# Optimization experiments

Measured on AMD Instinct MI355X. Metric: run time of the kernel, lower is better.

Reference implementation:

```python
import jax, jax.numpy as jnp
import numpy as np

DIM = 256
FEATURE_SCALE = 4
NMS_THRESHOLD = 8.0
PRE_NMS_TOPK = 2048
MAX_OUTPUT = 256
MIN_SCORE = 0.2


def conv3d_same(x, w, b):
    # x: [D,H,W,Cin], w: [3,3,3,Cin,Cout] -> [D,H,W,Cout], SAME padding (flax default)
    y = jax.lax.conv_general_dilated(
        x[None], w, window_strides=(1, 1, 1), padding="SAME",
        dimension_numbers=("NDHWC", "DHWIO", "NDHWC"))
    return y[0] + b


def setup_inputs() -> dict:
    key = jax.random.key(0)
    ks = jax.random.split(key, 8)
    D, H, W, C = 16, 64, 64, 256
    feature = jax.random.normal(ks[0], (D, H, W, C), jnp.float32)
    mask = jax.random.bernoulli(ks[1], 0.8, (D * FEATURE_SCALE, H * FEATURE_SCALE, W * FEATURE_SCALE))
    s3a = 1.0 / np.sqrt(27 * C)
    s3b = 1.0 / np.sqrt(27 * DIM)
    s1 = 1.0 / np.sqrt(DIM)
    w0 = jax.random.normal(ks[2], (3, 3, 3, C, DIM), jnp.float32) * s3a
    b0 = jnp.zeros((DIM,), jnp.float32)
    w1 = jax.random.normal(ks[3], (3, 3, 3, DIM, DIM), jnp.float32) * s3b
    b1 = jnp.zeros((DIM,), jnp.float32)
    w_logit = jax.random.normal(ks[4], (DIM, 1), jnp.float32) * s1
    b_logit = jnp.zeros((1,), jnp.float32)
    w_reg = jax.random.normal(ks[5], (DIM, 3), jnp.float32) * s1
    b_reg = jnp.zeros((3,), jnp.float32)
    return dict(feature=feature, mask=mask, w0=w0, b0=b0, w1=w1, b1=b1,
                w_logit=w_logit, b_logit=b_logit, w_reg=w_reg, b_reg=b_reg)


def reference(feature, mask, w0, b0, w1, b1, w_logit, b_logit, w_reg, b_reg):
    # ---- feature mixing: n_layers=2 of conv3d + gelu (flax gelu is approximate/tanh) ----
    x = jax.nn.gelu(conv3d_same(feature, w0, b0))
    x = jax.nn.gelu(conv3d_same(x, w1, b1))
    D, H, W = x.shape[:3]

    # ---- detection block: 1x1 convs are pointwise dense layers ----
    logits = (x @ w_logit + b_logit)[..., 0].reshape(-1)          # [N]
    regressions = (x @ w_reg + b_reg)                              # [D,H,W,3]
    ref_locs = (jnp.moveaxis(jnp.mgrid[:D, :H, :W], 0, -1) + 0.5) * FEATURE_SCALE
    pred_locs = (ref_locs + regressions * FEATURE_SCALE).reshape(-1, 3)  # [N,3]

    # ---- generate_predictions: sigmoid scores, pre-NMS top-k, greedy distance NMS ----
    scores = jax.nn.sigmoid(logits)
    top_scores, idx = jax.lax.top_k(scores, PRE_NMS_TOPK)          # sorted desc
    top_locs = pred_locs[idx]                                      # [K,3]
    d2 = ((top_locs[:, None, :] - top_locs[None, :, :]) ** 2).sum(-1)  # [K,K]
    th2 = NMS_THRESHOLD * NMS_THRESHOLD

    def step(suppressed, i):
        keep_i = (~suppressed[i]) & (top_scores[i] >= MIN_SCORE)
        suppressed = suppressed | (keep_i & (d2[i] < th2))
        return suppressed, keep_i

    _, keep = jax.lax.scan(step, jnp.zeros((PRE_NMS_TOPK,), bool), jnp.arange(PRE_NMS_TOPK))
    sel_scores = jnp.where(keep, top_scores, 0.0)
    out_scores, oidx = jax.lax.top_k(sel_scores, MAX_OUTPUT)       # [M]
    out_locs = top_locs[oidx]                                      # [M,3]

    # ---- mask gather: floor/clip/index, zero out-of-mask scores ----
    pli = jnp.floor(out_locs).astype(jnp.int32)
    bound = jnp.array(mask.shape, jnp.int32) - 1
    plc = jnp.clip(pli, 0, bound)
    in_range = (pli == plc).all(axis=1)
    masked = jnp.where(in_range, mask[plc[:, 0], plc[:, 1], plc[:, 2]], False)
    out_scores = jnp.where(masked, out_scores, 0.0)

    return jnp.concatenate([out_locs, out_scores[:, None]], axis=-1)  # [M,4] = (z,y,x,score)
```

## Files before the change

kernel.cpp:

```cpp
#include <hip/hip_runtime.h>
#include <math.h>

#define Dz 16
#define Hy 64
#define Wx 64
#define CHN 256
#define NVOX (Dz*Hy*Wx)
#define TOPK 2048
#define MAXOUT 256
#define CAND_CAP 4096
#define NBCAP 16
#define NHIST 65536

typedef __attribute__((ext_vector_type(8))) _Float16 h8;
typedef __attribute__((ext_vector_type(8))) unsigned short u16x8;
typedef __attribute__((ext_vector_type(4))) float f32x4;

__device__ __forceinline__ float gelu_tanh(float x) {
    return 0.5f*x*(1.0f + tanhf(0.7978845608028654f*(x + 0.044715f*x*x*x)));
}
__device__ __forceinline__ unsigned f2sort(float f) {
    unsigned u = __float_as_uint(f);
    return (u & 0x80000000u) ? ~u : (u | 0x80000000u);
}
__device__ __forceinline__ float sort2f(unsigned s) {
    unsigned u = (s & 0x80000000u) ? (s & 0x7fffffffu) : ~s;
    return __uint_as_float(u);
}

#define MFMA(d, a, b) d = __builtin_amdgcn_mfma_f32_16x16x32_f16(a, b, d, 0, 0, 0)

__global__ __launch_bounds__(256) void prep_kernel(const float* __restrict__ w0,
        const float* __restrict__ w1, u16x8* __restrict__ wpk0,
        u16x8* __restrict__ wpk1, unsigned* __restrict__ hist,
        unsigned* __restrict__ counter) {
    int b = blockIdx.x, t = threadIdx.x;
    if (b < 1728) {
        int id = b*256 + t;
        int l = (id >= 221184) ? 1 : 0;
        int r = id - l*221184;
        int lane = r & 63, ng = (r >> 6) & 15, kbg = (r >> 10) & 7, tp = r >> 13;
        const float* w = l ? w1 : w0;
        u16x8* dst = l ? wpk1 : wpk0;
        h8 hv, lv;
        #pragma unroll
        for (int j = 0; j < 8; ++j) {
            int k = kbg*32 + (lane >> 4)*8 + j;
            int co = ng*16 + (lane & 15);
            float v = w[((size_t)tp*CHN + k)*CHN + co];
            _Float16 h = (_Float16)v;
            hv[j] = h;
            lv[j] = (_Float16)(v - (float)h);
        }
        size_t base = (((size_t)(tp*8 + kbg)*16 + ng)*2)*64 + lane;
        dst[base]      = __builtin_bit_cast(u16x8, hv);
        dst[base + 64] = __builtin_bit_cast(u16x8, lv);
    } else {
        int zb = b - 1728;
        int i = zb*256 + t;
        hist[i] = 0u; hist[i + 16384] = 0u; hist[i + 32768] = 0u; hist[i + 49152] = 0u;
        if (zb == 0 && t == 0) counter[0] = 0u;
    }
}

template<int LAYER>
__global__ __launch_bounds__(512, 4) void conv_kernel(
        const float* __restrict__ fsrc,
        const unsigned short* __restrict__ hhi, const unsigned short* __restrict__ hlo,
        const u16x8* __restrict__ wpk, const float* __restrict__ bias,
        unsigned short* __restrict__ ohi, unsigned short* __restrict__ olo,
        const float* __restrict__ wlog, const float* __restrict__ blog,
        const float* __restrict__ wreg, const float* __restrict__ breg,
        float* __restrict__ locs, unsigned long long* __restrict__ keys,
        unsigned* __restrict__ hist) {
    __shared__ h8 sm[4224];
    const int tid = threadIdx.x;
    const int lane = tid & 63, w = tid >> 6;
    const int yo = w >> 2, wn = w & 3;
    const int lr = lane & 15, lg = lane >> 4;
    const int z = blockIdx.y, y0 = blockIdx.x*2;

    f32x4 acc[4][4];
    #pragma unroll
    for (int m = 0; m < 4; ++m)
        #pragma unroll
        for (int n = 0; n < 4; ++n) acc[m][n] = (f32x4){0.f,0.f,0.f,0.f};

    for (int dz = 0; dz < 3; ++dz) {
        const int zz = z + dz - 1;
        for (int kc = 0; kc < 4; ++kc) {
            __syncthreads();
            if (LAYER == 0) {
                for (int cidx = tid; cidx < 2112; cidx += 512) {
                    int cd = cidx & 7;
                    int rr = cidx >> 3;
                    int r = rr % 66, iy = rr / 66;
                    int ygl = y0 - 1 + iy, xin = r - 1;
                    h8 hv = {0,0,0,0,0,0,0,0}, lv = {0,0,0,0,0,0,0,0};
                    if (((unsigned)zz < (unsigned)Dz) & ((unsigned)ygl < (unsigned)Hy)
                        & ((unsigned)xin < (unsigned)Wx)) {
                        const float* s = fsrc + ((size_t)((zz*Hy + ygl)*Wx + xin))*CHN
                                              + kc*64 + cd*8;
                        float4 t0 = *(const float4*)s;
                        float4 t1 = *(const float4*)(s + 4);
                        float vv[8] = {t0.x,t0.y,t0.z,t0.w,t1.x,t1.y,t1.z,t1.w};
                        #pragma unroll
                        for (int j = 0; j < 8; ++j) {
                            _Float16 h = (_Float16)vv[j];
                            hv[j] = h;
                            lv[j] = (_Float16)(vv[j] - (float)h);
                        }
                    }
                    int sl = cd ^ (r & 7);
                    sm[(iy*66 + r)*8 + sl] = hv;
                    sm[2112 + (iy*66 + r)*8 + sl] = lv;
                }
            } else {
                for (int cidx = tid; cidx < 4224; cidx += 512) {
                    int c = cidx & 7;
                    int rr = cidx >> 3;
                    int r = rr % 66, tt = rr / 66;
                    int p = tt >> 2, iy = tt & 3;
                    int ygl = y0 - 1 + iy, xin = r - 1;
                    u16x8 v = {0,0,0,0,0,0,0,0};
                    if (((unsigned)zz < (unsigned)Dz) & ((unsigned)ygl < (unsigned)Hy)
                        & ((unsigned)xin < (unsigned)Wx)) {
                        const unsigned short* bp = p ? hlo : hhi;
                        v = *(const u16x8*)(bp + ((size_t)((zz*Hy + ygl)*Wx + xin))*CHN
                                               + kc*64 + (size_t)((c ^ (r & 7)))*8);
                    }
                    sm[cidx] = __builtin_bit_cast(h8, v);
                }
            }
            __syncthreads();
            for (int dy = 0; dy < 3; ++dy) {
                const int iyA = yo + dy;
                const h8* As = sm + iyA*528;
                #pragma unroll
                for (int dx = 0; dx < 3; ++dx) {
                    const int tap = (dz*3 + dy)*3 + dx;
                    #pragma unroll
                    for (int kb = 0; kb < 2; ++kb) {
                        const int kbg = kc*2 + kb;
                        const u16x8* wb = wpk + ((size_t)(tap*8 + kbg)*32 + wn*8)*64 + lane;
                        h8 bh[4];
                        #pragma unroll
                        for (int n = 0; n < 4; ++n)
                            bh[n] = __builtin_bit_cast(h8, wb[(size_t)n*128]);
                        #pragma unroll
                        for (int m = 0; m < 4; ++m) {
                            const int r = m*16 + lr + dx;
                            const int sl = (kb*4 + lg) ^ (r & 7);
                            h8 ah = As[r*8 + sl];
                            h8 al = As[2112 + r*8 + sl];
                            #pragma unroll
                            for (int n = 0; n < 4; ++n) {
                                MFMA(acc[m][n], ah, bh[n]);
                                MFMA(acc[m][n], al, bh[n]);
                            }
                        }
                        h8 bl[4];
                        #pragma unroll
                        for (int n = 0; n < 4; ++n)
                            bl[n] = __builtin_bit_cast(h8, wb[(size_t)n*128 + 64]);
                        #pragma unroll
                        for (int m = 0; m < 4; ++m) {
                            const int r = m*16 + lr + dx;
                            const int sl = (kb*4 + lg) ^ (r & 7);
                            h8 ah = As[r*8 + sl];
                            #pragma unroll
                            for (int n = 0; n < 4; ++n) MFMA(acc[m][n], ah, bl[n]);
                        }
                    }
                }
            }
        }
    }

    float bn[4];
    #pragma unroll
    for (int n = 0; n < 4; ++n) bn[n] = bias[wn*64 + n*16 + lr];

    if (LAYER == 0) {
        const int ygl = y0 + yo;
        #pragma unroll
        for (int m = 0; m < 4; ++m) {
            #pragma unroll
            for (int rg = 0; rg < 4; ++rg) {
                const int x = m*16 + lg*4 + rg;
                const size_t vbase = ((size_t)((z*Hy + ygl)*Wx + x))*CHN;
                #pragma unroll
                for (int n = 0; n < 4; ++n) {
                    const int co = wn*64 + n*16 + lr;
                    float g = gelu_tanh(acc[m][n][rg] + bn[n]);
                    _Float16 h = (_Float16)g;
                    _Float16 l = (_Float16)(g - (float)h);
                    ohi[vbase + co] = __builtin_bit_cast(unsigned short, h);
                    olo[vbase + co] = __builtin_bit_cast(unsigned short, l);
                }
            }
        }
    } else {
        float wl[4], wr0[4], wr1[4], wr2[4];
        #pragma unroll
        for (int n = 0; n < 4; ++n) {
            const int co = wn*64 + n*16 + lr;
            wl[n] = wlog[co];
            wr0[n] = wreg[co*3 + 0]; wr1[n] = wreg[co*3 + 1]; wr2[n] = wreg[co*3 + 2];
        }
        float p[4][16];
        #pragma unroll
        for (int c = 0; c < 4; ++c)
            #pragma unroll
            for (int xi = 0; xi < 16; ++xi) p[c][xi] = 0.f;
        #pragma unroll
        for (int m = 0; m < 4; ++m)
            #pragma unroll
            for (int rg = 0; rg < 4; ++rg) {
                const int xi = m*4 + rg;
                #pragma unroll
                for (int n = 0; n < 4; ++n) {
                    float g = gelu_tanh(acc[m][n][rg] + bn[n]);
                    p[0][xi] += g*wl[n];
                    p[1][xi] += g*wr0[n];
                    p[2][xi] += g*wr1[n];
                    p[3][xi] += g*wr2[n];
                }
            }
        #pragma unroll
        for (int st = 0; st < 4; ++st) {
            const int s = 1 << st;
            #pragma unroll
            for (int c = 0; c < 4; ++c)
                #pragma unroll
                for (int xi = 0; xi < 16; ++xi)
                    p[c][xi] += __shfl_xor(p[c][xi], s, 64);
        }
        __syncthreads();
        float* det = (float*)sm;
        if (lr == 0) {
            #pragma unroll
            for (int m = 0; m < 4; ++m)
                #pragma unroll
                for (int rg = 0; rg < 4; ++rg) {
                    const int x = m*16 + lg*4 + rg;
                    #pragma unroll
                    for (int c = 0; c < 4; ++c)
                        det[((yo*64 + x)*4 + c)*4 + wn] = p[c][m*4 + rg];
                }
        }
        __syncthreads();
        {
            const int yo2 = tid >> 8, x = (tid >> 2) & 63, chn = tid & 3;
            const float* dp = det + ((yo2*64 + x)*4 + chn)*4;
            float s = dp[0] + dp[1] + dp[2] + dp[3];
            const int ygl = y0 + yo2;
            const int vg = (z*Hy + ygl)*Wx + x;
            if (chn == 0) {
                float logit = s + blog[0];
                float score = 1.f/(1.f + expf(-logit));
                unsigned sb = f2sort(score);
                keys[vg] = ((unsigned long long)sb << 32)
                         | (unsigned long long)(0xFFFFFFFFu - (unsigned)vg);
                atomicAdd(&hist[sb >> 16], 1u);
            } else {
                float coord = (chn == 1) ? (float)z : (chn == 2) ? (float)ygl : (float)x;
                float loc = (coord + 0.5f)*4.0f + (s + breg[chn-1])*4.0f;
                locs[(size_t)vg*3 + (chn-1)] = loc;
            }
        }
    }
}

__global__ __launch_bounds__(1024) void find_cut_kernel(const unsigned* __restrict__ hist,
                                                        unsigned* __restrict__ cutp) {
    __shared__ unsigned ps[1024];
    __shared__ unsigned fs[64];
    __shared__ int sh_cb;
    __shared__ unsigned sh_acc;
    int t = threadIdx.x;
    unsigned s = 0;
    const unsigned* hp = hist + (size_t)t*64;
    for (int j = 0; j < 64; ++j) s += hp[j];
    ps[t] = s;
    __syncthreads();
    for (int off = 1; off < 1024; off <<= 1) {
        unsigned v = ps[t] + ((t + off < 1024) ? ps[t + off] : 0u);
        __syncthreads();
        ps[t] = v;
        __syncthreads();
    }
    if (ps[t] >= TOPK && (t == 1023 || ps[t+1] < TOPK)) {
        sh_cb = t; sh_acc = (t == 1023) ? 0u : ps[t+1];
    }
    __syncthreads();
    int cb = sh_cb; unsigned acc = sh_acc;
    if (t < 64) {
        unsigned f = acc;
        for (int u = t; u < 64; ++u) f += hist[(size_t)cb*64 + u];
        fs[t] = f;
    }
    __syncthreads();
    if (t < 64) {
        if (fs[t] >= TOPK && (t == 63 || fs[t+1] < TOPK))
            cutp[0] = ((unsigned)(cb*64 + t)) << 16;
    }
}

__global__ void compact_kernel(const unsigned long long* __restrict__ keys,
                               const unsigned* __restrict__ cutp,
                               unsigned* __restrict__ counter,
                               unsigned long long* __restrict__ cand) {
    int i = blockIdx.x*blockDim.x + threadIdx.x;
    unsigned thr = cutp[0];
    unsigned long long k = keys[i];
    if ((unsigned)(k >> 32) >= thr) {
        unsigned p = atomicAdd(counter, 1u);
        if (p < CAND_CAP) cand[p] = k;
    }
}

__global__ __launch_bounds__(128) void rank_kernel(const unsigned* __restrict__ counter,
        const unsigned long long* __restrict__ cand, const float* __restrict__ locs,
        float4* __restrict__ loc4G) {
    __shared__ unsigned long long kbuf[CAND_CAP];
    int t = threadIdx.x;
    int g = blockIdx.x*128 + t;
    int M = (int)*counter; if (M > CAND_CAP) M = CAND_CAP;
    for (int i = t; i < CAND_CAP; i += 128) kbuf[i] = (i < M) ? cand[i] : 0ull;
    __syncthreads();
    if (g >= M) return;
    unsigned long long mykey = kbuf[g];
    int rank = 0;
    for (int j = 0; j < M; ++j) rank += (kbuf[j] > mykey) ? 1 : 0;
    if (rank < TOPK) {
        unsigned idx = 0xFFFFFFFFu - (unsigned)(mykey & 0xFFFFFFFFull);
        float4 v;
        v.x = locs[(size_t)idx*3 + 0];
        v.y = locs[(size_t)idx*3 + 1];
        v.z = locs[(size_t)idx*3 + 2];
        v.w = sort2f((unsigned)(mykey >> 32));
        loc4G[rank] = v;
    }
}

__global__ __launch_bounds__(64) void nbr_kernel(const float4* __restrict__ loc4G,
        unsigned short* __restrict__ nbidx, unsigned char* __restrict__ nbcnt) {
    __shared__ float4 b4[TOPK];
    int t = threadIdx.x;
    int g = blockIdx.x*64 + t;
    for (int i = t; i < TOPK; i += 64) b4[i] = loc4G[i];
    __syncthreads();
    float4 me = b4[g];
    int cnt = 0;
    for (int j = 0; j < TOPK; ++j) {
        float4 o = b4[j];
        float dz = o.x - me.x, dy = o.y - me.y, dx = o.z - me.z;
        float d2 = dz*dz + dy*dy + dx*dx;
        if (d2 < 64.0f && j != g) {
            if (cnt < NBCAP) nbidx[(size_t)g*NBCAP + cnt] = (unsigned short)j;
            cnt++;
        }
    }
    nbcnt[g] = (unsigned char)min(cnt, 255);
}

__global__ __launch_bounds__(512) void nms_kernel(const float4* __restrict__ loc4G,
        const unsigned short* __restrict__ nbidx, const unsigned char* __restrict__ nbcnt,
        const int* __restrict__ mask, float* __restrict__ out) {
    __shared__ float4 p4[TOPK];
    __shared__ unsigned short snb[TOPK*NBCAP];
    __shared__ unsigned char scnt[TOPK];
    __shared__ unsigned char supf[TOPK];
    __shared__ unsigned char keepB[TOPK];
    __shared__ unsigned keepw[64];
    __shared__ int wpre[64];
    __shared__ int sh_nk;
    int t = threadIdx.x;
    for (int i = t; i < TOPK; i += 512) {
        p4[i] = loc4G[i]; scnt[i] = nbcnt[i]; supf[i] = 0; keepB[i] = 0;
    }
    for (int i = t; i < TOPK*NBCAP/8; i += 512)
        ((uint4*)snb)[i] = ((const uint4*)nbidx)[i];
    __syncthreads();
    if (t < 64) {
        const int l = t;
        float cz[32], cy[32], cx[32];
        #pragma unroll
        for (int j = 0; j < 32; ++j) {
            float4 v = p4[l*32 + j];
            cz[j] = v.x; cy[j] = v.y; cx[j] = v.z;
        }
        int myok = 0;
        #pragma unroll
        for (int j = 0; j < 32; ++j) myok += (p4[l*32 + j].w >= 0.2f) ? 1 : 0;
        #pragma unroll
        for (int s = 1; s < 64; s <<= 1) myok += __shfl_xor(myok, s, 64);
        const int NS = myok;
        int keeps = 0;
        for (int i = 0; i < NS; ++i) {
            bool kept = (supf[i] == 0);
            if (kept) {
                if (l == 0) keepB[i] = 1;
                ++keeps;
                const int cnt = scnt[i];
                if (cnt <= NBCAP) {
                    if (l < cnt) supf[snb[i*NBCAP + l]] = 1;
                } else {
                    float4 pv = p4[i];
                    #pragma unroll
                    for (int j = 0; j < 32; ++j) {
                        float dz = cz[j]-pv.x, dy = cy[j]-pv.y, dx = cx[j]-pv.z;
                        if (dz*dz + dy*dy + dx*dx < 64.0f) supf[l*32 + j] = 1;
                    }
                }
                asm volatile("s_waitcnt lgkmcnt(0)" ::: "memory");
                if (keeps >= MAXOUT) break;
            }
        }
    }
    __syncthreads();
    if (t < 64) {
        unsigned wmask = 0u;
        for (int j = 0; j < 32; ++j) wmask |= (keepB[t*32 + j] ? 1u : 0u) << j;
        keepw[t] = wmask;
    }
    __syncthreads();
    if (t < 64) {
        int p = 0;
        for (int j = 0; j < t; ++j) p += __popc(keepw[j]);
        wpre[t] = p;
        if (t == 63) sh_nk = p + __popc(keepw[63]);
    }
    __syncthreads();
    const int nk = sh_nk;
    for (int i = t; i < TOPK; i += 512) {
        unsigned w = keepw[i >> 5];
        bool kp = (w >> (i & 31)) & 1u;
        int rk = wpre[i >> 5] + __popc(w & ((1u << (i & 31)) - 1u));
        int slot = kp ? rk : (nk + (i - rk));
        if (slot < MAXOUT) {
            float4 v = p4[i];
            float lz = v.x, ly = v.y, lx = v.z;
            float sc = kp ? v.w : 0.f;
            int iz = (int)floorf(lz), iy = (int)floorf(ly), ix = (int)floorf(lx);
            int cz2 = min(max(iz,0),Dz*4-1), cy2 = min(max(iy,0),Hy*4-1), cx2 = min(max(ix,0),Wx*4-1);
            bool inr = (iz==cz2) && (iy==cy2) && (ix==cx2);
            float osc = (inr && mask[((size_t)cz2*(Hy*4) + cy2)*(Wx*4) + cx2] != 0) ? sc : 0.f;
            out[slot*4+0] = lz; out[slot*4+1] = ly; out[slot*4+2] = lx; out[slot*4+3] = osc;
        }
    }
}

extern "C" void kernel_launch(void* const* d_in, const int* in_sizes, int n_in,
                              void* d_out, int out_size, void* d_ws, size_t ws_size,
                              hipStream_t stream) {
    const float* feature = (const float*)d_in[0];
    const int*   mask    = (const int*)d_in[1];
    const float* w0   = (const float*)d_in[2];
    const float* b0   = (const float*)d_in[3];
    const float* w1   = (const float*)d_in[4];
    const float* b1   = (const float*)d_in[5];
    const float* wlog = (const float*)d_in[6];
    const float* blog = (const float*)d_in[7];
    const float* wreg = (const float*)d_in[8];
    const float* breg = (const float*)d_in[9];

    char* ws = (char*)d_ws;
    size_t off = 0;
    unsigned short* h1hi = (unsigned short*)(ws + off); off += (size_t)NVOX*CHN*2;
    unsigned short* h1lo = (unsigned short*)(ws + off); off += (size_t)NVOX*CHN*2;
    u16x8* wpk0 = (u16x8*)(ws + off);               off += (size_t)442368*16;
    u16x8* wpk1 = (u16x8*)(ws + off);               off += (size_t)442368*16;
    unsigned long long* keys = (unsigned long long*)(ws + off); off += (size_t)NVOX*8;
    float* locs = (float*)(ws + off);               off += (size_t)NVOX*3*4;
    unsigned* hist = (unsigned*)(ws + off);         off += (size_t)NHIST*4;
    unsigned* counter = (unsigned*)(ws + off);      off += 256;
    unsigned* cutp = counter + 1;
    unsigned long long* cand = (unsigned long long*)(ws + off); off += (size_t)CAND_CAP*8;
    float4* loc4G = (float4*)(ws + off);            off += (size_t)TOPK*16;
    unsigned short* nbidx = (unsigned short*)(ws + off); off += (size_t)TOPK*NBCAP*2;
    unsigned char* nbcnt = (unsigned char*)(ws + off);   off += (size_t)TOPK;
    if (ws_size < off) return;

    prep_kernel<<<1792, 256, 0, stream>>>(w0, w1, wpk0, wpk1, hist, counter);
    dim3 cgrid(Hy/2, Dz);
    conv_kernel<0><<<cgrid, 512, 0, stream>>>(feature, nullptr, nullptr, wpk0, b0,
                                              h1hi, h1lo,
                                              nullptr, nullptr, nullptr, nullptr,
                                              nullptr, nullptr, nullptr);
    conv_kernel<1><<<cgrid, 512, 0, stream>>>(nullptr, h1hi, h1lo, wpk1, b1,
                                              nullptr, nullptr,
                                              wlog, blog, wreg, breg,
                                              locs, keys, hist);
    find_cut_kernel<<<1, 1024, 0, stream>>>(hist, cutp);
    compact_kernel<<<NVOX/256, 256, 0, stream>>>(keys, cutp, counter, cand);
    rank_kernel<<<CAND_CAP/128, 128, 0, stream>>>(counter, cand, locs, loc4G);
    nbr_kernel<<<TOPK/64, 64, 0, stream>>>(loc4G, nbidx, nbcnt);
    nms_kernel<<<1, 512, 0, stream>>>(loc4G, nbidx, nbcnt, mask, (float*)d_out);
}
```

Measured before the change: 1.382 ms.

## Double-buffer conv input tiles in LDS and widen blocks to 1024 threads

The conv kernels now use two LDS buffers. The next (dz, kc) input chunk is prefetched into registers while MFMAs run on the current buffer, then written to the other buffer, so only one barrier is needed per stage. Blocks grow to 1024 threads (16 waves), each wave covering 32 output channels instead of 64. This halves per-wave accumulators but doubles LDS use and doubles how often each A fragment is re-read across waves. The detection reduction is adjusted to sum over 8 channel groups.

After: 1.373 ms (median of 2 runs). Within noise of the previous version (-0.6%).

```diff
diff --git a/kernel.cpp b/kernel.cpp
--- a/kernel.cpp
+++ b/kernel.cpp
@@ -63,8 +63,51 @@
     }
 }
 
+__device__ __forceinline__ u16x8 ld1(int cidx, const unsigned short* __restrict__ hhi,
+        const unsigned short* __restrict__ hlo, int zz, bool zok, int y0, int kc) {
+    int c = cidx & 7, rr = cidx >> 3;
+    int r = rr % 66, tt = rr / 66;
+    int p = tt >> 2, iy = tt & 3;
+    int ygl = y0 - 1 + iy, xin = r - 1;
+    u16x8 v = {0,0,0,0,0,0,0,0};
+    if (zok & ((unsigned)ygl < (unsigned)Hy) & ((unsigned)xin < (unsigned)Wx)) {
+        const unsigned short* bp = p ? hlo : hhi;
+        v = *(const u16x8*)(bp + ((size_t)((zz*Hy + ygl)*Wx + xin))*CHN
+                            + kc*64 + (size_t)(c ^ (r & 7))*8);
+    }
+    return v;
+}
+__device__ __forceinline__ void ld0(int cidx, const float* __restrict__ fsrc,
+        int zz, bool zok, int y0, int kc, float4& va, float4& vb) {
+    int cd = cidx & 7, rr = cidx >> 3;
+    int r = rr % 66, iy = rr / 66;
+    int ygl = y0 - 1 + iy, xin = r - 1;
+    va = make_float4(0.f,0.f,0.f,0.f); vb = va;
+    if (zok & ((unsigned)ygl < (unsigned)Hy) & ((unsigned)xin < (unsigned)Wx)) {
+        const float* s = fsrc + ((size_t)((zz*Hy + ygl)*Wx + xin))*CHN + kc*64 + cd*8;
+        va = *(const float4*)s;
+        vb = *(const float4*)(s + 4);
+    }
+}
+__device__ __forceinline__ void st0(h8* __restrict__ dst, int cidx,
+                                    float4 va, float4 vb) {
+    int cd = cidx & 7, rr = cidx >> 3;
+    int r = rr % 66, iy = rr / 66;
+    float vv[8] = {va.x,va.y,va.z,va.w,vb.x,vb.y,vb.z,vb.w};
+    h8 hv, lv;
+    #pragma unroll
+    for (int j = 0; j < 8; ++j) {
+        _Float16 h = (_Float16)vv[j];
+        hv[j] = h;
+        lv[j] = (_Float16)(vv[j] - (float)h);
+    }
+    int sl = cd ^ (r & 7);
+    dst[(iy*66 + r)*8 + sl] = hv;
+    dst[2112 + (iy*66 + r)*8 + sl] = lv;
+}
+
 template<int LAYER>
-__global__ __launch_bounds__(512, 4) void conv_kernel(
+__global__ __launch_bounds__(1024) void conv_kernel(
         const float* __restrict__ fsrc,
         const unsigned short* __restrict__ hhi, const unsigned short* __restrict__ hlo,
         const u16x8* __restrict__ wpk, const float* __restrict__ bias,
@@ -73,116 +116,116 @@
         const float* __restrict__ wreg, const float* __restrict__ breg,
         float* __restrict__ locs, unsigned long long* __restrict__ keys,
         unsigned* __restrict__ hist) {
-    __shared__ h8 sm[4224];
+    __shared__ h8 sm[8448];
     const int tid = threadIdx.x;
     const int lane = tid & 63, w = tid >> 6;
-    const int yo = w >> 2, wn = w & 3;
+    const int mw = w >> 3, wn = w & 7;
     const int lr = lane & 15, lg = lane >> 4;
     const int z = blockIdx.y, y0 = blockIdx.x*2;
 
-    f32x4 acc[4][4];
+    f32x4 acc[4][2];
     #pragma unroll
     for (int m = 0; m < 4; ++m)
         #pragma unroll
-        for (int n = 0; n < 4; ++n) acc[m][n] = (f32x4){0.f,0.f,0.f,0.f};
-
-    for (int dz = 0; dz < 3; ++dz) {
-        const int zz = z + dz - 1;
-        for (int kc = 0; kc < 4; ++kc) {
-            __syncthreads();
-            if (LAYER == 0) {
-                for (int cidx = tid; cidx < 2112; cidx += 512) {
-                    int cd = cidx & 7;
-                    int rr = cidx >> 3;
-                    int r = rr % 66, iy = rr / 66;
-                    int ygl = y0 - 1 + iy, xin = r - 1;
-                    h8 hv = {0,0,0,0,0,0,0,0}, lv = {0,0,0,0,0,0,0,0};
-                    if (((unsigned)zz < (unsigned)Dz) & ((unsigned)ygl < (unsigned)Hy)
-                        & ((unsigned)xin < (unsigned)Wx)) {
-                        const float* s = fsrc + ((size_t)((zz*Hy + ygl)*Wx + xin))*CHN
-                                              + kc*64 + cd*8;
-                        float4 t0 = *(const float4*)s;
-                        float4 t1 = *(const float4*)(s + 4);
-                        float vv[8] = {t0.x,t0.y,t0.z,t0.w,t1.x,t1.y,t1.z,t1.w};
-                        #pragma unroll
-                        for (int j = 0; j < 8; ++j) {
-                            _Float16 h = (_Float16)vv[j];
-                            hv[j] = h;
-                            lv[j] = (_Float16)(vv[j] - (float)h);
-                        }
+        for (int n = 0; n < 2; ++n) acc[m][n] = (f32x4){0.f,0.f,0.f,0.f};
+
+    u16x8 s1a, s1b, s1c, s1d, s1e;
+    float4 s0a0, s0a1, s0b0, s0b1, s0c0, s0c1;
+
+#define STAGE_LOAD(DZ2, KC2) do {                                              \
+    const int zz2_ = z + (DZ2) - 1;                                            \
+    const bool zok2_ = (unsigned)zz2_ < (unsigned)Dz;                          \
+    if constexpr (LAYER == 0) {                                                \
+        ld0(tid,        fsrc, zz2_, zok2_, y0, (KC2), s0a0, s0a1);             \
+        ld0(1024 + tid, fsrc, zz2_, zok2_, y0, (KC2), s0b0, s0b1);             \
+        if (tid < 64) ld0(2048 + tid, fsrc, zz2_, zok2_, y0, (KC2), s0c0, s0c1);\
+    } else {                                                                   \
+        s1a = ld1(tid,        hhi, hlo, zz2_, zok2_, y0, (KC2));               \
+        s1b = ld1(1024 + tid, hhi, hlo, zz2_, zok2_, y0, (KC2));               \
+        s1c = ld1(2048 + tid, hhi, hlo, zz2_, zok2_, y0, (KC2));               \
+        s1d = ld1(3072 + tid, hhi, hlo, zz2_, zok2_, y0, (KC2));               \
+        if (tid < 128) s1e = ld1(4096 + tid, hhi, hlo, zz2_, zok2_, y0, (KC2));\
+    }                                                                          \
+    __builtin_amdgcn_sched_barrier(0);                                         \
+} while (0)
+
+#define STAGE_WRITE(PAR) do {                                                  \
+    h8* dst_ = sm + (PAR)*4224;                                                \
+    if constexpr (LAYER == 0) {                                                \
+        st0(dst_, tid,        s0a0, s0a1);                                     \
+        st0(dst_, 1024 + tid, s0b0, s0b1);                                     \
+        if (tid < 64) st0(dst_, 2048 + tid, s0c0, s0c1);                       \
+    } else {                                                                   \
+        dst_[tid]        = __builtin_bit_cast(h8, s1a);                        \
+        dst_[1024 + tid] = __builtin_bit_cast(h8, s1b);                        \
+        dst_[2048 + tid] = __builtin_bit_cast(h8, s1c);                        \
+        dst_[3072 + tid] = __builtin_bit_cast(h8, s1d);                        \
+        if (tid < 128) dst_[4096 + tid] = __builtin_bit_cast(h8, s1e);         \
+    }                                                                          \
+} while (0)
+
+    STAGE_LOAD(0, 0);
+    STAGE_WRITE(0);
+    __syncthreads();
+
+    for (int k = 0; k < 12; ++k) {
+        const int dz = k >> 2, kc = k & 3;
+        const int par = k & 1;
+        if (k < 11) {
+            const int k2 = k + 1;
+            STAGE_LOAD(k2 >> 2, k2 & 3);
+        }
+        const h8* As0 = sm + par*4224;
+        for (int dy = 0; dy < 3; ++dy) {
+            const int iyA = mw + dy;
+            const h8* As = As0 + iyA*528;
+            #pragma unroll
+            for (int dx = 0; dx < 3; ++dx) {
+                const int tap = (dz*3 + dy)*3 + dx;
+                #pragma unroll
+                for (int kb = 0; kb < 2; ++kb) {
+                    const int kbg = kc*2 + kb;
+                    const u16x8* wb = wpk + ((size_t)(tap*8 + kbg)*32 + wn*4)*64 + lane;
+                    h8 bh0 = __builtin_bit_cast(h8, wb[0]);
+                    h8 bh1 = __builtin_bit_cast(h8, wb[128]);
+                    #pragma unroll
+                    for (int m = 0; m < 4; ++m) {
+                        const int r = m*16 + lr + dx;
+                        const int sl = (kb*4 + lg) ^ (r & 7);
+                        h8 ah = As[r*8 + sl];
+                        h8 al = As[2112 + r*8 + sl];
+                        MFMA(acc[m][0], ah, bh0);
+                        MFMA(acc[m][0], al, bh0);
+                        MFMA(acc[m][1], ah, bh1);
+                        MFMA(acc[m][1], al, bh1);
                     }
-                    int sl = cd ^ (r & 7);
-                    sm[(iy*66 + r)*8 + sl] = hv;
-                    sm[2112 + (iy*66 + r)*8 + sl] = lv;
-                }
-            } else {
-                for (int cidx = tid; cidx < 4224; cidx += 512) {
-                    int c = cidx & 7;
-                    int rr = cidx >> 3;
-                    int r = rr % 66, tt = rr / 66;
-                    int p = tt >> 2, iy = tt & 3;
-                    int ygl = y0 - 1 + iy, xin = r - 1;
-                    u16x8 v = {0,0,0,0,0,0,0,0};
-                    if (((unsigned)zz < (unsigned)Dz) & ((unsigned)ygl < (unsigned)Hy)
-                        & ((unsigned)xin < (unsigned)Wx)) {
-                        const unsigned short* bp = p ? hlo : hhi;
-                        v = *(const u16x8*)(bp + ((size_t)((zz*Hy + ygl)*Wx + xin))*CHN
-                                               + kc*64 + (size_t)((c ^ (r & 7)))*8);
-                    }
-                    sm[cidx] = __builtin_bit_cast(h8, v);
-                }
-            }
-            __syncthreads();
-            for (int dy = 0; dy < 3; ++dy) {
-                const int iyA = yo + dy;
-                const h8* As = sm + iyA*528;
-                #pragma unroll
-                for (int dx = 0; dx < 3; ++dx) {
-                    const int tap = (dz*3 + dy)*3 + dx;
+                    h8 bl0 = __builtin_bit_cast(h8, wb[64]);
+                    h8 bl1 = __builtin_bit_cast(h8, wb[192]);
                     #pragma unroll
-                    for (int kb = 0; kb < 2; ++kb) {
-                        const int kbg = kc*2 + kb;
-                        const u16x8* wb = wpk + ((size_t)(tap*8 + kbg)*32 + wn*8)*64 + lane;
-                        h8 bh[4];
-                        #pragma unroll
-                        for (int n = 0; n < 4; ++n)
-                            bh[n] = __builtin_bit_cast(h8, wb[(size_t)n*128]);
-                        #pragma unroll
-                        for (int m = 0; m < 4; ++m) {
-                            const int r = m*16 + lr + dx;
-                            const int sl = (kb*4 + lg) ^ (r & 7);
-                            h8 ah = As[r*8 + sl];
-                            h8 al = As[2112 + r*8 + sl];
-                            #pragma unroll
-                            for (int n = 0; n < 4; ++n) {
-                                MFMA(acc[m][n], ah, bh[n]);
-                                MFMA(acc[m][n], al, bh[n]);
-                            }
-                        }
-                        h8 bl[4];
-                        #pragma unroll
-                        for (int n = 0; n < 4; ++n)
-                            bl[n] = __builtin_bit_cast(h8, wb[(size_t)n*128 + 64]);
-                        #pragma unroll
-                        for (int m = 0; m < 4; ++m) {
-                            const int r = m*16 + lr + dx;
-                            const int sl = (kb*4 + lg) ^ (r & 7);
-                            h8 ah = As[r*8 + sl];
-                            #pragma unroll
-                            for (int n = 0; n < 4; ++n) MFMA(acc[m][n], ah, bl[n]);
-                        }
+                    for (int m = 0; m < 4; ++m) {
+                        const int r = m*16 + lr + dx;
+                        const int sl = (kb*4 + lg) ^ (r & 7);
+                        h8 ah = As[r*8 + sl];
+                        MFMA(acc[m][0], ah, bl0);
+                        MFMA(acc[m][1], ah, bl1);
                     }
                 }
             }
         }
-    }
-
-    float bn[4];
+        if (k < 11) {
+            STAGE_WRITE((k + 1) & 1);
+            __syncthreads();
+        }
+    }
+#undef STAGE_LOAD
+#undef STAGE_WRITE
+
+    float bn[2];
     #pragma unroll
-    for (int n = 0; n < 4; ++n) bn[n] = bias[wn*64 + n*16 + lr];
+    for (int n = 0; n < 2; ++n) bn[n] = bias[wn*32 + n*16 + lr];
 
     if (LAYER == 0) {
-        const int ygl = y0 + yo;
+        const int ygl = y0 + mw;
         #pragma unroll
         for (int m = 0; m < 4; ++m) {
             #pragma unroll
@@ -190,8 +233,8 @@
                 const int x = m*16 + lg*4 + rg;
                 const size_t vbase = ((size_t)((z*Hy + ygl)*Wx + x))*CHN;
                 #pragma unroll
-                for (int n = 0; n < 4; ++n) {
-                    const int co = wn*64 + n*16 + lr;
+                for (int n = 0; n < 2; ++n) {
+                    const int co = wn*32 + n*16 + lr;
                     float g = gelu_tanh(acc[m][n][rg] + bn[n]);
                     _Float16 h = (_Float16)g;
                     _Float16 l = (_Float16)(g - (float)h);
@@ -201,10 +244,10 @@
             }
         }
     } else {
-        float wl[4], wr0[4], wr1[4], wr2[4];
-        #pragma unroll
-        for (int n = 0; n < 4; ++n) {
-            const int co = wn*64 + n*16 + lr;
+        float wl[2], wr0[2], wr1[2], wr2[2];
+        #pragma unroll
+        for (int n = 0; n < 2; ++n) {
+            const int co = wn*32 + n*16 + lr;
             wl[n] = wlog[co];
             wr0[n] = wreg[co*3 + 0]; wr1[n] = wreg[co*3 + 1]; wr2[n] = wreg[co*3 + 2];
         }
@@ -219,7 +262,7 @@
             for (int rg = 0; rg < 4; ++rg) {
                 const int xi = m*4 + rg;
                 #pragma unroll
-                for (int n = 0; n < 4; ++n) {
+                for (int n = 0; n < 2; ++n) {
                     float g = gelu_tanh(acc[m][n][rg] + bn[n]);
                     p[0][xi] += g*wl[n];
                     p[1][xi] += g*wr0[n];
@@ -246,15 +289,15 @@
                     const int x = m*16 + lg*4 + rg;
                     #pragma unroll
                     for (int c = 0; c < 4; ++c)
-                        det[((yo*64 + x)*4 + c)*4 + wn] = p[c][m*4 + rg];
+                        det[((mw*64 + x)*4 + c)*8 + wn] = p[c][m*4 + rg];
                 }
         }
         __syncthreads();
-        {
-            const int yo2 = tid >> 8, x = (tid >> 2) & 63, chn = tid & 3;
-            const float* dp = det + ((yo2*64 + x)*4 + chn)*4;
-            float s = dp[0] + dp[1] + dp[2] + dp[3];
-            const int ygl = y0 + yo2;
+        if (tid < 512) {
+            const int vox = tid >> 2, chn = tid & 3;
+            const float* dp = det + ((size_t)(vox*4 + chn))*8;
+            float s = dp[0] + dp[1] + dp[2] + dp[3] + dp[4] + dp[5] + dp[6] + dp[7];
+            const int ygl = y0 + (vox >> 6), x = vox & 63;
             const int vg = (z*Hy + ygl)*Wx + x;
             if (chn == 0) {
                 float logit = s + blog[0];
@@ -485,14 +528,14 @@
 
     prep_kernel<<<1792, 256, 0, stream>>>(w0, w1, wpk0, wpk1, hist, counter);
     dim3 cgrid(Hy/2, Dz);
-    conv_kernel<0><<<cgrid, 512, 0, stream>>>(feature, nullptr, nullptr, wpk0, b0,
-                                              h1hi, h1lo,
-                                              nullptr, nullptr, nullptr, nullptr,
-                                              nullptr, nullptr, nullptr);
-    conv_kernel<1><<<cgrid, 512, 0, stream>>>(nullptr, h1hi, h1lo, wpk1, b1,
-                                              nullptr, nullptr,
-                                              wlog, blog, wreg, breg,
-                                              locs, keys, hist);
+    conv_kernel<0><<<cgrid, 1024, 0, stream>>>(feature, nullptr, nullptr, wpk0, b0,
+                                               h1hi, h1lo,
+                                               nullptr, nullptr, nullptr, nullptr,
+                                               nullptr, nullptr, nullptr);
+    conv_kernel<1><<<cgrid, 1024, 0, stream>>>(nullptr, h1hi, h1lo, wpk1, b1,
+                                               nullptr, nullptr,
+                                               wlog, blog, wreg, breg,
+                                               locs, keys, hist);
     find_cut_kernel<<<1, 1024, 0, stream>>>(hist, cutp);
     compact_kernel<<<NVOX/256, 256, 0, stream>>>(keys, cutp, counter, cand);
     rank_kernel<<<CAND_CAP/128, 128, 0, stream>>>(counter, cand, locs, loc4G);
```

## Switch conv MFMA to 32x32x16 tiles with per-wave channel slabs

Applied to the files above, without the earlier changes.

Replaces the 16x16x32 fp16 MFMA tiling with 32x32x16 instructions: each wave now owns 32 output channels across all 128 voxels of the block, and the weight packing is reorganized to match. This aims to raise MFMA throughput and cut per-wave weight loads. In exchange, LDS activation reads per wave grow somewhat and the layer-2 detection head does longer shuffle reductions per element.

New measurement: 1.476 ms. 1.07x slower.

```diff
diff --git a/kernel.cpp b/kernel.cpp
--- a/kernel.cpp
+++ b/kernel.cpp
@@ -14,7 +14,7 @@
 
 typedef __attribute__((ext_vector_type(8))) _Float16 h8;
 typedef __attribute__((ext_vector_type(8))) unsigned short u16x8;
-typedef __attribute__((ext_vector_type(4))) float f32x4;
+typedef __attribute__((ext_vector_type(16))) float f32x16;
 
 __device__ __forceinline__ float gelu_tanh(float x) {
     return 0.5f*x*(1.0f + tanhf(0.7978845608028654f*(x + 0.044715f*x*x*x)));
@@ -28,7 +28,7 @@
     return __uint_as_float(u);
 }
 
-#define MFMA(d, a, b) d = __builtin_amdgcn_mfma_f32_16x16x32_f16(a, b, d, 0, 0, 0)
+#define MFMA32(d, a, b) d = __builtin_amdgcn_mfma_f32_32x32x16_f16(a, b, d, 0, 0, 0)
 
 __global__ __launch_bounds__(256) void prep_kernel(const float* __restrict__ w0,
         const float* __restrict__ w1, u16x8* __restrict__ wpk0,
@@ -39,20 +39,20 @@
         int id = b*256 + t;
         int l = (id >= 221184) ? 1 : 0;
         int r = id - l*221184;
-        int lane = r & 63, ng = (r >> 6) & 15, kbg = (r >> 10) & 7, tp = r >> 13;
+        int lane = r & 63, ng = (r >> 6) & 7, kg = (r >> 9) & 15, tp = r >> 13;
         const float* w = l ? w1 : w0;
         u16x8* dst = l ? wpk1 : wpk0;
         h8 hv, lv;
         #pragma unroll
         for (int j = 0; j < 8; ++j) {
-            int k = kbg*32 + (lane >> 4)*8 + j;
-            int co = ng*16 + (lane & 15);
+            int k = kg*16 + (lane >> 5)*8 + j;
+            int co = ng*32 + (lane & 31);
             float v = w[((size_t)tp*CHN + k)*CHN + co];
             _Float16 h = (_Float16)v;
             hv[j] = h;
             lv[j] = (_Float16)(v - (float)h);
         }
-        size_t base = (((size_t)(tp*8 + kbg)*16 + ng)*2)*64 + lane;
+        size_t base = (((size_t)(tp*16 + kg)*8 + ng)*2)*64 + lane;
         dst[base]      = __builtin_bit_cast(u16x8, hv);
         dst[base + 64] = __builtin_bit_cast(u16x8, lv);
     } else {
@@ -75,16 +75,15 @@
         unsigned* __restrict__ hist) {
     __shared__ h8 sm[4224];
     const int tid = threadIdx.x;
-    const int lane = tid & 63, w = tid >> 6;
-    const int yo = w >> 2, wn = w & 3;
-    const int lr = lane & 15, lg = lane >> 4;
+    const int lane = tid & 63, wn = tid >> 6;
+    const int l31 = lane & 31, lhi = lane >> 5;
     const int z = blockIdx.y, y0 = blockIdx.x*2;
 
-    f32x4 acc[4][4];
+    f32x16 acc[4];
     #pragma unroll
     for (int m = 0; m < 4; ++m)
         #pragma unroll
-        for (int n = 0; n < 4; ++n) acc[m][n] = (f32x4){0.f,0.f,0.f,0.f};
+        for (int q = 0; q < 16; ++q) acc[m][q] = 0.f;
 
     for (int dz = 0; dz < 3; ++dz) {
         const int zz = z + dz - 1;
@@ -134,127 +133,89 @@
             }
             __syncthreads();
             for (int dy = 0; dy < 3; ++dy) {
-                const int iyA = yo + dy;
-                const h8* As = sm + iyA*528;
                 #pragma unroll
                 for (int dx = 0; dx < 3; ++dx) {
                     const int tap = (dz*3 + dy)*3 + dx;
                     #pragma unroll
-                    for (int kb = 0; kb < 2; ++kb) {
-                        const int kbg = kc*2 + kb;
-                        const u16x8* wb = wpk + ((size_t)(tap*8 + kbg)*32 + wn*8)*64 + lane;
-                        h8 bh[4];
-                        #pragma unroll
-                        for (int n = 0; n < 4; ++n)
-                            bh[n] = __builtin_bit_cast(h8, wb[(size_t)n*128]);
+                    for (int k16 = 0; k16 < 4; ++k16) {
+                        const int kg = kc*4 + k16;
+                        const u16x8* wb = wpk
+                            + ((size_t)((tap*16 + kg)*8 + wn)*2)*64 + lane;
+                        h8 bh = __builtin_bit_cast(h8, wb[0]);
+                        h8 bl = __builtin_bit_cast(h8, wb[64]);
+                        const int cb = k16*2 + lhi;
+                        h8 ah[4], al[4];
                         #pragma unroll
                         for (int m = 0; m < 4; ++m) {
-                            const int r = m*16 + lr + dx;
-                            const int sl = (kb*4 + lg) ^ (r & 7);
-                            h8 ah = As[r*8 + sl];
-                            h8 al = As[2112 + r*8 + sl];
-                            #pragma unroll
-                            for (int n = 0; n < 4; ++n) {
-                                MFMA(acc[m][n], ah, bh[n]);
-                                MFMA(acc[m][n], al, bh[n]);
-                            }
+                            const int iyA = (m >> 1) + dy;
+                            const int r = (m & 1)*32 + l31 + dx;
+                            const int sl = cb ^ (r & 7);
+                            const int base = (iyA*66 + r)*8 + sl;
+                            ah[m] = sm[base];
+                            al[m] = sm[2112 + base];
                         }
-                        h8 bl[4];
                         #pragma unroll
-                        for (int n = 0; n < 4; ++n)
-                            bl[n] = __builtin_bit_cast(h8, wb[(size_t)n*128 + 64]);
+                        for (int m = 0; m < 4; ++m) MFMA32(acc[m], ah[m], bh);
                         #pragma unroll
-                        for (int m = 0; m < 4; ++m) {
-                            const int r = m*16 + lr + dx;
-                            const int sl = (kb*4 + lg) ^ (r & 7);
-                            h8 ah = As[r*8 + sl];
-                            #pragma unroll
-                            for (int n = 0; n < 4; ++n) MFMA(acc[m][n], ah, bl[n]);
-                        }
+                        for (int m = 0; m < 4; ++m) MFMA32(acc[m], al[m], bh);
+                        #pragma unroll
+                        for (int m = 0; m < 4; ++m) MFMA32(acc[m], ah[m], bl);
                     }
                 }
             }
         }
     }
 
-    float bn[4];
-    #pragma unroll
-    for (int n = 0; n < 4; ++n) bn[n] = bias[wn*64 + n*16 + lr];
+    const int co = wn*32 + l31;
+    const float bco = bias[co];
 
     if (LAYER == 0) {
-        const int ygl = y0 + yo;
+        #pragma unroll
+        for (int m = 0; m < 4; ++m) {
+            const int ygl = y0 + (m >> 1);
+            #pragma unroll
+            for (int q = 0; q < 16; ++q) {
+                const int x = (m & 1)*32 + (q & 3) + 8*(q >> 2) + 4*lhi;
+                float g = gelu_tanh(acc[m][q] + bco);
+                _Float16 h = (_Float16)g;
+                _Float16 lo = (_Float16)(g - (float)h);
+                const size_t vbase = ((size_t)((z*Hy + ygl)*Wx + x))*CHN + co;
+                ohi[vbase] = __builtin_bit_cast(unsigned short, h);
+                olo[vbase] = __builtin_bit_cast(unsigned short, lo);
+            }
+        }
+    } else {
+        const float wl = wlog[co];
+        const float wr0 = wreg[co*3 + 0], wr1 = wreg[co*3 + 1], wr2 = wreg[co*3 + 2];
+        __syncthreads();
+        float* det = (float*)sm;
         #pragma unroll
         for (int m = 0; m < 4; ++m) {
             #pragma unroll
-            for (int rg = 0; rg < 4; ++rg) {
-                const int x = m*16 + lg*4 + rg;
-                const size_t vbase = ((size_t)((z*Hy + ygl)*Wx + x))*CHN;
+            for (int q = 0; q < 16; ++q) {
+                float g = gelu_tanh(acc[m][q] + bco);
+                float p0 = g*wl, p1 = g*wr0, p2 = g*wr1, p3 = g*wr2;
                 #pragma unroll
-                for (int n = 0; n < 4; ++n) {
-                    const int co = wn*64 + n*16 + lr;
-                    float g = gelu_tanh(acc[m][n][rg] + bn[n]);
-                    _Float16 h = (_Float16)g;
-                    _Float16 l = (_Float16)(g - (float)h);
-                    ohi[vbase + co] = __builtin_bit_cast(unsigned short, h);
-                    olo[vbase + co] = __builtin_bit_cast(unsigned short, l);
-                }
-            }
-        }
-    } else {
-        float wl[4], wr0[4], wr1[4], wr2[4];
-        #pragma unroll
-        for (int n = 0; n < 4; ++n) {
-            const int co = wn*64 + n*16 + lr;
-            wl[n] = wlog[co];
-            wr0[n] = wreg[co*3 + 0]; wr1[n] = wreg[co*3 + 1]; wr2[n] = wreg[co*3 + 2];
-        }
-        float p[4][16];
-        #pragma unroll
-        for (int c = 0; c < 4; ++c)
-            #pragma unroll
-            for (int xi = 0; xi < 16; ++xi) p[c][xi] = 0.f;
-        #pragma unroll
-        for (int m = 0; m < 4; ++m)
-            #pragma unroll
-            for (int rg = 0; rg < 4; ++rg) {
-                const int xi = m*4 + rg;
-                #pragma unroll
-                for (int n = 0; n < 4; ++n) {
-                    float g = gelu_tanh(acc[m][n][rg] + bn[n]);
-                    p[0][xi] += g*wl[n];
-                    p[1][xi] += g*wr0[n];
-                    p[2][xi] += g*wr1[n];
-                    p[3][xi] += g*wr2[n];
-                }
-            }
-        #pragma unroll
-        for (int st = 0; st < 4; ++st) {
-            const int s = 1 << st;
-            #pragma unroll
-            for (int c = 0; c < 4; ++c)
-                #pragma unroll
-                for (int xi = 0; xi < 16; ++xi)
-                    p[c][xi] += __shfl_xor(p[c][xi], s, 64);
-        }
-        __syncthreads();
-        float* det = (float*)sm;
-        if (lr == 0) {
-            #pragma unroll
-            for (int m = 0; m < 4; ++m)
-                #pragma unroll
-                for (int rg = 0; rg < 4; ++rg) {
-                    const int x = m*16 + lg*4 + rg;
-                    #pragma unroll
-                    for (int c = 0; c < 4; ++c)
-                        det[((yo*64 + x)*4 + c)*4 + wn] = p[c][m*4 + rg];
-                }
+                for (int s = 1; s < 32; s <<= 1) {
+                    p0 += __shfl_xor(p0, s, 64);
+                    p1 += __shfl_xor(p1, s, 64);
+                    p2 += __shfl_xor(p2, s, 64);
+                    p3 += __shfl_xor(p3, s, 64);
+                }
+                if (l31 == 0) {
+                    const int x = (m & 1)*32 + (q & 3) + 8*(q >> 2) + 4*lhi;
+                    const int iy = m >> 1;
+                    float* dp = det + ((size_t)((iy*64 + x)*4))*8 + wn;
+                    dp[0] = p0; dp[8] = p1; dp[16] = p2; dp[24] = p3;
+                }
+            }
         }
         __syncthreads();
         {
-            const int yo2 = tid >> 8, x = (tid >> 2) & 63, chn = tid & 3;
-            const float* dp = det + ((yo2*64 + x)*4 + chn)*4;
-            float s = dp[0] + dp[1] + dp[2] + dp[3];
-            const int ygl = y0 + yo2;
+            const int vox = tid >> 2, chn = tid & 3;
+            const float* dp = det + ((size_t)(vox*4 + chn))*8;
+            float s = dp[0] + dp[1] + dp[2] + dp[3] + dp[4] + dp[5] + dp[6] + dp[7];
+            const int ygl = y0 + (vox >> 6), x = vox & 63;
             const int vg = (z*Hy + ygl)*Wx + x;
             if (chn == 0) {
                 float logit = s + blog[0];
```

## Merge post-conv selection and NMS into one kernel, swizzle conv block order

Applied to the files above, without the earlier changes.

Folds the five post-processing kernels (cut finding, compaction, ranking, neighbour search, NMS) into a single 1024-thread tail kernel that keeps candidates, locations and neighbour lists in shared memory. This removes four kernel launches and the global round-trips between them. The conv grid becomes a 1D 512-block launch with a swizzled block-to-(z,y) mapping, meant to improve cache locality across concurrently scheduled blocks. In exchange, compaction over 65536 voxels, the O(M^2) ranking and the O(K^2) neighbour search now all run on one workgroup instead of many, which may serialize work.

Measured after the change: 1.638 ms. 18.6% more time.

```diff
diff --git a/kernel.cpp b/kernel.cpp
--- a/kernel.cpp
+++ b/kernel.cpp
@@ -32,8 +32,7 @@
 
 __global__ __launch_bounds__(256) void prep_kernel(const float* __restrict__ w0,
         const float* __restrict__ w1, u16x8* __restrict__ wpk0,
-        u16x8* __restrict__ wpk1, unsigned* __restrict__ hist,
-        unsigned* __restrict__ counter) {
+        u16x8* __restrict__ wpk1, unsigned* __restrict__ hist) {
     int b = blockIdx.x, t = threadIdx.x;
     if (b < 1728) {
         int id = b*256 + t;
@@ -59,7 +58,6 @@
         int zb = b - 1728;
         int i = zb*256 + t;
         hist[i] = 0u; hist[i + 16384] = 0u; hist[i + 32768] = 0u; hist[i + 49152] = 0u;
-        if (zb == 0 && t == 0) counter[0] = 0u;
     }
 }
 
@@ -78,7 +76,9 @@
     const int lane = tid & 63, w = tid >> 6;
     const int yo = w >> 2, wn = w & 3;
     const int lr = lane & 15, lg = lane >> 4;
-    const int z = blockIdx.y, y0 = blockIdx.x*2;
+    const int bid = blockIdx.x;
+    const int swz = (bid & 7)*64 + (bid >> 3);
+    const int z = swz >> 5, y0 = (swz & 31)*2;
 
     f32x4 acc[4][4];
     #pragma unroll
@@ -272,102 +272,12 @@
     }
 }
 
-__global__ __launch_bounds__(1024) void find_cut_kernel(const unsigned* __restrict__ hist,
-                                                        unsigned* __restrict__ cutp) {
+__global__ __launch_bounds__(1024) void tail_kernel(const unsigned* __restrict__ hist,
+        const unsigned long long* __restrict__ keys, const float* __restrict__ locs,
+        const int* __restrict__ mask, float* __restrict__ out) {
     __shared__ unsigned ps[1024];
     __shared__ unsigned fs[64];
-    __shared__ int sh_cb;
-    __shared__ unsigned sh_acc;
-    int t = threadIdx.x;
-    unsigned s = 0;
-    const unsigned* hp = hist + (size_t)t*64;
-    for (int j = 0; j < 64; ++j) s += hp[j];
-    ps[t] = s;
-    __syncthreads();
-    for (int off = 1; off < 1024; off <<= 1) {
-        unsigned v = ps[t] + ((t + off < 1024) ? ps[t + off] : 0u);
-        __syncthreads();
-        ps[t] = v;
-        __syncthreads();
-    }
-    if (ps[t] >= TOPK && (t == 1023 || ps[t+1] < TOPK)) {
-        sh_cb = t; sh_acc = (t == 1023) ? 0u : ps[t+1];
-    }
-    __syncthreads();
-    int cb = sh_cb; unsigned acc = sh_acc;
-    if (t < 64) {
-        unsigned f = acc;
-        for (int u = t; u < 64; ++u) f += hist[(size_t)cb*64 + u];
-        fs[t] = f;
-    }
-    __syncthreads();
-    if (t < 64) {
-        if (fs[t] >= TOPK && (t == 63 || fs[t+1] < TOPK))
-            cutp[0] = ((unsigned)(cb*64 + t)) << 16;
-    }
-}
-
-__global__ void compact_kernel(const unsigned long long* __restrict__ keys,
-                               const unsigned* __restrict__ cutp,
-                               unsigned* __restrict__ counter,
-                               unsigned long long* __restrict__ cand) {
-    int i = blockIdx.x*blockDim.x + threadIdx.x;
-    unsigned thr = cutp[0];
-    unsigned long long k = keys[i];
-    if ((unsigned)(k >> 32) >= thr) {
-        unsigned p = atomicAdd(counter, 1u);
-        if (p < CAND_CAP) cand[p] = k;
-    }
-}
-
-__global__ __launch_bounds__(128) void rank_kernel(const unsigned* __restrict__ counter,
-        const unsigned long long* __restrict__ cand, const float* __restrict__ locs,
-        float4* __restrict__ loc4G) {
-    __shared__ unsigned long long kbuf[CAND_CAP];
-    int t = threadIdx.x;
-    int g = blockIdx.x*128 + t;
-    int M = (int)*counter; if (M > CAND_CAP) M = CAND_CAP;
-    for (int i = t; i < CAND_CAP; i += 128) kbuf[i] = (i < M) ? cand[i] : 0ull;
-    __syncthreads();
-    if (g >= M) return;
-    unsigned long long mykey = kbuf[g];
-    int rank = 0;
-    for (int j = 0; j < M; ++j) rank += (kbuf[j] > mykey) ? 1 : 0;
-    if (rank < TOPK) {
-        unsigned idx = 0xFFFFFFFFu - (unsigned)(mykey & 0xFFFFFFFFull);
-        float4 v;
-        v.x = locs[(size_t)idx*3 + 0];
-        v.y = locs[(size_t)idx*3 + 1];
-        v.z = locs[(size_t)idx*3 + 2];
-        v.w = sort2f((unsigned)(mykey >> 32));
-        loc4G[rank] = v;
-    }
-}
-
-__global__ __launch_bounds__(64) void nbr_kernel(const float4* __restrict__ loc4G,
-        unsigned short* __restrict__ nbidx, unsigned char* __restrict__ nbcnt) {
-    __shared__ float4 b4[TOPK];
-    int t = threadIdx.x;
-    int g = blockIdx.x*64 + t;
-    for (int i = t; i < TOPK; i += 64) b4[i] = loc4G[i];
-    __syncthreads();
-    float4 me = b4[g];
-    int cnt = 0;
-    for (int j = 0; j < TOPK; ++j) {
-        float4 o = b4[j];
-        float dz = o.x - me.x, dy = o.y - me.y, dx = o.z - me.z;
-        float d2 = dz*dz + dy*dy + dx*dx;
-        if (d2 < 64.0f && j != g) {
-            if (cnt < NBCAP) nbidx[(size_t)g*NBCAP + cnt] = (unsigned short)j;
-            cnt++;
-        }
-    }
-    nbcnt[g] = (unsigned char)min(cnt, 255);
-}
-
-__global__ __launch_bounds__(512) void nms_kernel(const float4* __restrict__ loc4G,
-        const unsigned short* __restrict__ nbidx, const unsigned char* __restrict__ nbcnt,
-        const int* __restrict__ mask, float* __restrict__ out) {
+    __shared__ unsigned long long cand[CAND_CAP];
     __shared__ float4 p4[TOPK];
     __shared__ unsigned short snb[TOPK*NBCAP];
     __shared__ unsigned char scnt[TOPK];
@@ -375,14 +285,87 @@
     __shared__ unsigned char keepB[TOPK];
     __shared__ unsigned keepw[64];
     __shared__ int wpre[64];
-    __shared__ int sh_nk;
-    int t = threadIdx.x;
-    for (int i = t; i < TOPK; i += 512) {
-        p4[i] = loc4G[i]; scnt[i] = nbcnt[i]; supf[i] = 0; keepB[i] = 0;
-    }
-    for (int i = t; i < TOPK*NBCAP/8; i += 512)
-        ((uint4*)snb)[i] = ((const uint4*)nbidx)[i];
+    __shared__ int sh_cb, sh_nk;
+    __shared__ unsigned sh_acc, sh_cut, sh_cnt;
+    const int t = threadIdx.x;
+
+    {
+        unsigned s = 0;
+        const unsigned* hp = hist + (size_t)t*64;
+        for (int j = 0; j < 64; ++j) s += hp[j];
+        ps[t] = s;
+        if (t == 0) sh_cnt = 0u;
+        __syncthreads();
+        for (int off = 1; off < 1024; off <<= 1) {
+            unsigned v = ps[t] + ((t + off < 1024) ? ps[t + off] : 0u);
+            __syncthreads();
+            ps[t] = v;
+            __syncthreads();
+        }
+        if (ps[t] >= TOPK && (t == 1023 || ps[t+1] < TOPK)) {
+            sh_cb = t; sh_acc = (t == 1023) ? 0u : ps[t+1];
+        }
+        __syncthreads();
+        int cb = sh_cb; unsigned acc = sh_acc;
+        if (t < 64) {
+            unsigned f = acc;
+            for (int u = t; u < 64; ++u) f += hist[(size_t)cb*64 + u];
+            fs[t] = f;
+        }
+        __syncthreads();
+        if (t < 64) {
+            if (fs[t] >= TOPK && (t == 63 || fs[t+1] < TOPK))
+                sh_cut = ((unsigned)(cb*64 + t)) << 16;
+        }
+        __syncthreads();
+    }
+
+    {
+        const unsigned cut = sh_cut;
+        for (int i = t; i < NVOX; i += 1024) {
+            unsigned long long k = keys[i];
+            if ((unsigned)(k >> 32) >= cut) {
+                unsigned p = atomicAdd(&sh_cnt, 1u);
+                if (p < CAND_CAP) cand[p] = k;
+            }
+        }
+        __syncthreads();
+    }
+    const int M = (sh_cnt > CAND_CAP) ? CAND_CAP : (int)sh_cnt;
+
+    for (int g = t; g < M; g += 1024) {
+        unsigned long long mykey = cand[g];
+        int rank = 0;
+        for (int j = 0; j < M; ++j) rank += (cand[j] > mykey) ? 1 : 0;
+        if (rank < TOPK) {
+            unsigned idx = 0xFFFFFFFFu - (unsigned)(mykey & 0xFFFFFFFFull);
+            float4 v;
+            v.x = locs[(size_t)idx*3 + 0];
+            v.y = locs[(size_t)idx*3 + 1];
+            v.z = locs[(size_t)idx*3 + 2];
+            v.w = sort2f((unsigned)(mykey >> 32));
+            p4[rank] = v;
+        }
+    }
+    for (int i = t; i < TOPK; i += 1024) { supf[i] = 0; keepB[i] = 0; }
     __syncthreads();
+
+    for (int g = t; g < TOPK; g += 1024) {
+        float4 me = p4[g];
+        int cnt = 0;
+        for (int j = 0; j < TOPK; ++j) {
+            float4 o = p4[j];
+            float dz = o.x - me.x, dy = o.y - me.y, dx = o.z - me.z;
+            float d2 = dz*dz + dy*dy + dx*dx;
+            if (d2 < 64.0f && j != g) {
+                if (cnt < NBCAP) snb[g*NBCAP + cnt] = (unsigned short)j;
+                cnt++;
+            }
+        }
+        scnt[g] = (unsigned char)min(cnt, 255);
+    }
+    __syncthreads();
+
     if (t < 64) {
         const int l = t;
         float cz[32], cy[32], cx[32];
@@ -433,8 +416,9 @@
         if (t == 63) sh_nk = p + __popc(keepw[63]);
     }
     __syncthreads();
+
     const int nk = sh_nk;
-    for (int i = t; i < TOPK; i += 512) {
+    for (int i = t; i < TOPK; i += 1024) {
         unsigned w = keepw[i >> 5];
         bool kp = (w >> (i & 31)) & 1u;
         int rk = wpre[i >> 5] + __popc(w & ((1u << (i & 31)) - 1u));
@@ -475,27 +459,16 @@
     unsigned long long* keys = (unsigned long long*)(ws + off); off += (size_t)NVOX*8;
     float* locs = (float*)(ws + off);               off += (size_t)NVOX*3*4;
     unsigned* hist = (unsigned*)(ws + off);         off += (size_t)NHIST*4;
-    unsigned* counter = (unsigned*)(ws + off);      off += 256;
-    unsigned* cutp = counter + 1;
-    unsigned long long* cand = (unsigned long long*)(ws + off); off += (size_t)CAND_CAP*8;
-    float4* loc4G = (float4*)(ws + off);            off += (size_t)TOPK*16;
-    unsigned short* nbidx = (unsigned short*)(ws + off); off += (size_t)TOPK*NBCAP*2;
-    unsigned char* nbcnt = (unsigned char*)(ws + off);   off += (size_t)TOPK;
     if (ws_size < off) return;
 
-    prep_kernel<<<1792, 256, 0, stream>>>(w0, w1, wpk0, wpk1, hist, counter);
-    dim3 cgrid(Hy/2, Dz);
-    conv_kernel<0><<<cgrid, 512, 0, stream>>>(feature, nullptr, nullptr, wpk0, b0,
-                                              h1hi, h1lo,
-                                              nullptr, nullptr, nullptr, nullptr,
-                                              nullptr, nullptr, nullptr);
-    conv_kernel<1><<<cgrid, 512, 0, stream>>>(nullptr, h1hi, h1lo, wpk1, b1,
-                                              nullptr, nullptr,
-                                              wlog, blog, wreg, breg,
-                                              locs, keys, hist);
-    find_cut_kernel<<<1, 1024, 0, stream>>>(hist, cutp);
-    compact_kernel<<<NVOX/256, 256, 0, stream>>>(keys, cutp, counter, cand);
-    rank_kernel<<<CAND_CAP/128, 128, 0, stream>>>(counter, cand, locs, loc4G);
-    nbr_kernel<<<TOPK/64, 64, 0, stream>>>(loc4G, nbidx, nbcnt);
-    nms_kernel<<<1, 512, 0, stream>>>(loc4G, nbidx, nbcnt, mask, (float*)d_out);
-}
+    prep_kernel<<<1792, 256, 0, stream>>>(w0, w1, wpk0, wpk1, hist);
+    conv_kernel<0><<<512, 512, 0, stream>>>(feature, nullptr, nullptr, wpk0, b0,
+                                            h1hi, h1lo,
+                                            nullptr, nullptr, nullptr, nullptr,
+                                            nullptr, nullptr, nullptr);
+    conv_kernel<1><<<512, 512, 0, stream>>>(nullptr, h1hi, h1lo, wpk1, b1,
+                                            nullptr, nullptr,
+                                            wlog, blog, wreg, breg,
+                                            locs, keys, hist);
+    tail_kernel<<<1, 1024, 0, stream>>>(hist, keys, locs, mask, (float*)d_out);
+}
```
